# Kernel tuning notes

Measured on AMD Instinct MI355X. Metric: run time of the kernel, lower is better.

The kernel has to match this reference:

```python
import jax, jax.numpy as jnp
import numpy as np

B, S, D = 4, 2048, 512
H, DK, DV = 8, 64, 64

def setup_inputs() -> dict:
    key = jax.random.key(0)
    ks = jax.random.split(key, 11)
    s = 0.02
    return {
        "q_in": jax.random.normal(ks[0], (B, S, D), jnp.float32),
        "k_in": jax.random.normal(ks[1], (B, S, D), jnp.float32),
        "v_in": jax.random.normal(ks[2], (B, S, D), jnp.float32),
        "Wq": jax.random.normal(ks[3], (H, D, DK), jnp.float32) * s,
        "bq": jax.random.normal(ks[4], (H, DK), jnp.float32) * s,
        "Wk": jax.random.normal(ks[5], (H, D, DK), jnp.float32) * s,
        "bk": jax.random.normal(ks[6], (H, DK), jnp.float32) * s,
        "Wv": jax.random.normal(ks[7], (H, D, DV), jnp.float32) * s,
        "bv": jax.random.normal(ks[8], (H, DV), jnp.float32) * s,
        "Wo": jax.random.normal(ks[9], (H * DV, D), jnp.float32) * s,
        "bo": jax.random.normal(ks[10], (D,), jnp.float32) * s,
    }


def reference(q_in, k_in, v_in, Wq, bq, Wk, bk, Wv, bv, Wo, bo):
    # Per-head Q/K/V projections, batched over heads (same math as the
    # original Python loop over SingleAttention heads).
    q = jnp.einsum("bsd,hdk->bhsk", q_in, Wq) + bq[None, :, None, :]   # [B,H,S,DK]
    k = jnp.einsum("bsd,hdk->bhsk", k_in, Wk) + bk[None, :, None, :]   # [B,H,S,DK]
    v = jnp.einsum("bsd,hdv->bhsv", v_in, Wv) + bv[None, :, None, :]   # [B,H,S,DV]
    scale = 1.0 / jnp.sqrt(jnp.float32(DK))
    scores = jnp.einsum("bhqk,bhsk->bhqs", q, k) * scale               # [B,H,S,S]
    attn = jax.nn.softmax(scores, axis=-1)
    out = jnp.einsum("bhqs,bhsv->bhqv", attn, v)                        # [B,H,S,DV]
    # concat heads along feature dim: [B,S,H*DV]
    concat = out.transpose(0, 2, 1, 3).reshape(B, S, H * DV)
    return concat @ Wo + bo                                             # [B,S,D]
```

## Files before the change

kernel.cpp:

```cpp
#include <hip/hip_runtime.h>
#include <hip/hip_bf16.h>

using bf16 = __hip_bfloat16;
typedef short short8  __attribute__((ext_vector_type(8)));
typedef short short4v __attribute__((ext_vector_type(4)));
typedef float float4v __attribute__((ext_vector_type(4)));
typedef float f32x16  __attribute__((ext_vector_type(16)));
typedef unsigned int uint4v __attribute__((ext_vector_type(4)));

#define MFMA_BF16   __builtin_amdgcn_mfma_f32_16x16x32_bf16
#define MFMA32_BF16 __builtin_amdgcn_mfma_f32_32x32x16_bf16

#define B_  4
#define S_  2048
#define D_  512
#define H_  8
#define DK_ 64

__device__ __forceinline__ short f2bf(float f) {
  bf16 h = __float2bfloat16(f);
  return *reinterpret_cast<short*>(&h);
}

__device__ __forceinline__ unsigned cvtpk(float lo, float hi) {
  unsigned r;
  asm("v_cvt_pk_bf16_f32 %0, %1, %2" : "=v"(r) : "v"(lo), "v"(hi));
  return r;
}

__device__ __forceinline__ void plswap(unsigned& a, unsigned& b) {
  asm("v_permlane32_swap_b32 %0, %1" : "+v"(a), "+v"(b));
}

__device__ __forceinline__ short8 mk8(unsigned v0, unsigned v1, unsigned v2,
                                      unsigned v3) {
  uint4v u;
  u[0] = v0; u[1] = v1; u[2] = v2; u[3] = v3;
  return __builtin_bit_cast(short8, u);
}

#define GLL(g, l) __builtin_amdgcn_global_load_lds(                        \
      (const __attribute__((address_space(1))) void*)(g),                  \
      (__attribute__((address_space(3))) void*)(l), 16, 0, 0)

__global__ __launch_bounds__(256)
void prep(const float* __restrict__ qin, const float* __restrict__ kin,
          const float* __restrict__ vin, short* __restrict__ Xb,
          const float* __restrict__ Wq, const float* __restrict__ Wk,
          const float* __restrict__ Wv, const float* __restrict__ Wo,
          short* __restrict__ WqT, short* __restrict__ WkT,
          short* __restrict__ WvT, short* __restrict__ WoT) {
  __shared__ float tile[64 * 65];
  const int bid = blockIdx.x, tid = threadIdx.x;
  const size_t NTOK = (size_t)B_ * S_ * D_;

  if (bid < 6144) {
    const int z = bid >> 11, blk = bid & 2047;
    const float* src = (z == 0) ? qin : (z == 1) ? kin : vin;
    short* dst = Xb + (size_t)z * NTOK;
    const size_t base = ((size_t)blk * 256 + tid) * 8;
    float4v f0 = *(const float4v*)&src[base];
    float4v f1 = *(const float4v*)&src[base + 4];
    short8 s;
#pragma unroll
    for (int j = 0; j < 4; j++) { s[j] = f2bf(f0[j]); s[j + 4] = f2bf(f1[j]); }
    *(short8*)&dst[base] = s;
    return;
  }

  const int tw = bid - 6144;
  const int mat = tw >> 6, t = tw & 63;
  const float* W = (mat == 0) ? Wq : (mat == 1) ? Wk : (mat == 2) ? Wv : Wo;
  short* T       = (mat == 0) ? WqT : (mat == 1) ? WkT : (mat == 2) ? WvT : WoT;

  size_t sbase, ss, dbase;
  if (mat < 3) {
    int hh = t >> 3, d0 = (t & 7) * 64;
    sbase = (size_t)hh * 32768 + (size_t)d0 * 64;
    ss = 64;
    dbase = (size_t)hh * 64 * 512 + d0;
  } else {
    int n0 = (t >> 3) * 64, k0 = (t & 7) * 64;
    sbase = (size_t)k0 * 512 + n0;
    ss = 512;
    dbase = (size_t)n0 * 512 + k0;
  }

  {
    int r = tid >> 2, c0 = (tid & 3) * 16;
#pragma unroll
    for (int j = 0; j < 4; j++)
      *(float4v*)&tile[r * 65 + c0 + j * 4] =
          *(const float4v*)&W[sbase + (size_t)r * ss + c0 + j * 4];
  }
  __syncthreads();
  {
    int c = tid >> 2, r0 = (tid & 3) * 16;
#pragma unroll
    for (int j = 0; j < 2; j++) {
      short8 s;
#pragma unroll
      for (int u = 0; u < 8; u++) s[u] = f2bf(tile[(r0 + j * 8 + u) * 65 + c]);
      *(short8*)&T[dbase + (size_t)c * 512 + r0 + j * 8] = s;
    }
  }
}

__device__ __forceinline__ void gemm_core3(const short* __restrict__ A,
                                           const short* __restrict__ Bt,
                                           int m0, int n0,
                                           short* ABs,
                                           float4v acc[4][4]) {
  const int tid  = threadIdx.x;
  const int lane = tid & 63, wave = tid >> 6;
  const int quad = lane >> 4, l16 = lane & 15;
  const int wm = (wave >> 1) * 64, wn = (wave & 1) * 64;

  auto stage = [&](int buf, int k0) {
#pragma unroll
    for (int i = 0; i < 4; i++) {
      int q = (wave * 4 + i) * 64 + lane;
      int row = q >> 3, p = q & 7;
      int c = p ^ (row & 7);
      const short* src = (c < 4)
          ? &A [(size_t)(m0 + row) * 512 + k0 + c * 8]
          : &Bt[(size_t)(n0 + row) * 512 + k0 + (c - 4) * 8];
      GLL(src, &ABs[buf * 8192 + (wave * 4 + i) * 512]);
    }
  };
  auto comp = [&](int buf) {
    short8 af[4], bfr[4];
#pragma unroll
    for (int mi = 0; mi < 4; mi++) {
      int row = wm + mi * 16 + l16;
      af[mi] = *(short8*)&ABs[buf * 8192 + row * 64 + ((quad ^ (row & 7)) << 3)];
    }
#pragma unroll
    for (int ni = 0; ni < 4; ni++) {
      int row = wn + ni * 16 + l16;
      bfr[ni] = *(short8*)&ABs[buf * 8192 + row * 64 +
                               (((4 + quad) ^ (row & 7)) << 3)];
    }
#pragma unroll
    for (int mi = 0; mi < 4; mi++)
#pragma unroll
      for (int ni = 0; ni < 4; ni++)
        acc[mi][ni] = MFMA_BF16(af[mi], bfr[ni], acc[mi][ni], 0, 0, 0);
  };

  stage(0, 0);
  __syncthreads();
#pragma unroll
  for (int k = 0; k < 512; k += 64) {
    stage(1, k + 32);
    comp(0);
    __syncthreads();
    if (k + 64 < 512) stage(0, k + 64);
    comp(1);
    __syncthreads();
  }
}

__global__ __launch_bounds__(256, 4)
void qkv_gemm(const short* __restrict__ Xb,
              const short* __restrict__ WqT, const short* __restrict__ WkT,
              const short* __restrict__ WvT,
              const float* __restrict__ bq, const float* __restrict__ bk,
              const float* __restrict__ bv,
              short* __restrict__ Qp, short* __restrict__ Kp,
              short* __restrict__ Vt) {
  __shared__ __align__(16) short ABs[2 * 8192];
  const int m0 = blockIdx.x * 128, n0 = blockIdx.y * 128;
  const int z = blockIdx.z;
  const size_t NTOK = (size_t)B_ * S_ * D_;
  const short* A    = Xb + (size_t)z * NTOK;
  const short* Bt   = (z == 0) ? WqT : (z == 1) ? WkT : WvT;
  const float* bias = (z == 0) ? bq  : (z == 1) ? bk  : bv;
  const float scale = (z == 0) ? 0.125f * 1.44269504088896f : 1.0f;

  float4v acc[4][4];
#pragma unroll
  for (int mi = 0; mi < 4; mi++)
#pragma unroll
    for (int ni = 0; ni < 4; ni++) acc[mi][ni] = (float4v){0.f, 0.f, 0.f, 0.f};

  gemm_core3(A, Bt, m0, n0, ABs, acc);

  const int lane = threadIdx.x & 63, wave = threadIdx.x >> 6;
  const int quad = lane >> 4, l16 = lane & 15;
  const int wm = (wave >> 1) * 64, wn = (wave & 1) * 64;

  if (z < 2) {
    short* out = (z == 0) ? Qp : Kp;
#pragma unroll
    for (int mi = 0; mi < 4; mi++) {
      int m = m0 + wm + mi * 16 + quad * 4;
      int b = m >> 11, s = m & 2047;
#pragma unroll
      for (int ni = 0; ni < 4; ni++) {
        int n = n0 + wn + ni * 16 + l16;
        int h = n >> 6, dk = n & 63;
        float bb = bias[n];
        size_t base = (((size_t)b * H_ + h) * S_ + s) * 64 + dk;
#pragma unroll
        for (int r = 0; r < 4; r++)
          out[base + (size_t)r * 64] = f2bf((acc[mi][ni][r] + bb) * scale);
      }
    }
  } else {
#pragma unroll
    for (int mi = 0; mi < 4; mi++) {
      int m = m0 + wm + mi * 16 + quad * 4;
      int b = m >> 11, s = m & 2047;
#pragma unroll
      for (int ni = 0; ni < 4; ni++) {
        int n = n0 + wn + ni * 16 + l16;
        int h = n >> 6, v = n & 63;
        float bb = bias[n];
        short4v pk;
#pragma unroll
        for (int r = 0; r < 4; r++) pk[r] = f2bf(acc[mi][ni][r] + bb);
        *(short4v*)&Vt[(((size_t)b * H_ + h) * 64 + v) * S_ + s] = pk;
      }
    }
  }
}

__global__ __launch_bounds__(512, 4)
void attn_kernel(const short* __restrict__ Qp, const short* __restrict__ Kp,
                 const short* __restrict__ Vt, short* __restrict__ Ao) {
  __shared__ __align__(16) short sh[32768];

  const int orig = blockIdx.y * gridDim.x + blockIdx.x;
  const int lb = (orig & 7) * 64 + (orig >> 3);
  const int qt = lb & 15, bh = lb >> 4;
  const int b = bh >> 3, h = bh & 7;

  const int tid = threadIdx.x;
  const int lane = tid & 63, wave = tid >> 6;
  const int wg = wave & 3, half = wave >> 2;
  const int l31 = lane & 31, hi = lane >> 5, s7 = l31 & 7;

  const short* Qb = Qp + (size_t)bh * S_ * 64;
  const short* Kb = Kp + (size_t)bh * S_ * 64 + (size_t)half * 1024 * 64;
  const short* Vb = Vt + (size_t)bh * 64 * S_;

  short8 qf[4];
  {
    const short* qrow = Qb + (size_t)(qt * 128 + wg * 32 + l31) * 64;
#pragma unroll
    for (int w = 0; w < 4; w++)
      qf[w] = *(const short8*)&qrow[w * 16 + hi * 8];
  }

  const int slot0 = wg * 128 + lane;
  const int kr0 = slot0 >> 3, kc0 = slot0 & 7;
  const int kr1 = kr0 + 8;
  const short* kg0 = Kb + (size_t)kr0 * 64 + ((kc0 ^ (kr0 & 7)) << 3);
  const short* kg1 = Kb + (size_t)kr1 * 64 + ((kc0 ^ (kr1 & 7)) << 3);
  const short* vg0 = Vb + (size_t)kr0 * S_ + half * 1024 + ((kc0 ^ (kr0 & 7)) << 3);
  const short* vg1 = Vb + (size_t)kr1 * S_ + half * 1024 + ((kc0 ^ (kr1 & 7)) << 3);

  short* Kbase = sh;
  short* Vbase = sh + 16384;

  f32x16 acc0, acc1;
#pragma unroll
  for (int r = 0; r < 16; r++) { acc0[r] = 0.f; acc1[r] = 0.f; }
  float ls0 = 0.f, ls1 = 0.f;

  {
    short* kd = Kbase + (half * 2) * 4096 + wg * 1024;
    short* vd = Vbase + (half * 2) * 4096 + wg * 1024;
    GLL(kg0, kd); GLL(kg1, kd + 512);
    GLL(vg0, vd); GLL(vg1, vd + 512);
  }
  __syncthreads();

  for (int t = 0; t < 16; t++) {
    const int cur = t & 1;
    if (t < 15) {
      short* kd = Kbase + (half * 2 + (cur ^ 1)) * 4096 + wg * 1024;
      short* vd = Vbase + (half * 2 + (cur ^ 1)) * 4096 + wg * 1024;
      GLL(kg0 + (size_t)(t + 1) * 4096, kd);
      GLL(kg1 + (size_t)(t + 1) * 4096, kd + 512);
      GLL(vg0 + (size_t)(t + 1) * 64, vd);
      GLL(vg1 + (size_t)(t + 1) * 64, vd + 512);
    }
    const short* kb = Kbase + (half * 2 + cur) * 4096;
    const short* vs = Vbase + (half * 2 + cur) * 4096;

#pragma unroll
    for (int kt = 0; kt < 2; kt++) {
      f32x16 sa;
#pragma unroll
      for (int r = 0; r < 16; r++) sa[r] = 0.f;
      __builtin_amdgcn_s_setprio(1);
#pragma unroll
      for (int w = 0; w < 4; w++) {
        short8 kf = *(const short8*)&kb[(kt * 32 + l31) * 64 +
                                        (((2 * w + hi) ^ s7) << 3)];
        sa = MFMA32_BF16(kf, qf[w], sa, 0, 0, 0);
      }
      __builtin_amdgcn_s_setprio(0);

      float pv[16];
#pragma unroll
      for (int r = 0; r < 16; r++) pv[r] = exp2f(sa[r]);
#pragma unroll
      for (int r = 0; r < 8; r++) { ls0 += pv[r]; ls1 += pv[r + 8]; }

      unsigned a0 = cvtpk(pv[0], pv[1]),  b0 = cvtpk(pv[4], pv[5]);
      plswap(a0, b0);
      unsigned c0 = cvtpk(pv[2], pv[3]),  d0 = cvtpk(pv[6], pv[7]);
      plswap(c0, d0);
      short8 pa0 = mk8(a0, c0, b0, d0);
      unsigned a1 = cvtpk(pv[8], pv[9]),  b1 = cvtpk(pv[12], pv[13]);
      plswap(a1, b1);
      unsigned c1 = cvtpk(pv[10], pv[11]), d1 = cvtpk(pv[14], pv[15]);
      plswap(c1, d1);
      short8 pa1 = mk8(a1, c1, b1, d1);

      __builtin_amdgcn_s_setprio(1);
      {
        const int kw0 = kt * 2, kw1 = kt * 2 + 1;
        short8 v00 = *(const short8*)&vs[l31 * 64 + (((2 * kw0 + hi) ^ s7) << 3)];
        short8 v10 = *(const short8*)&vs[(32 + l31) * 64 + (((2 * kw0 + hi) ^ s7) << 3)];
        acc0 = MFMA32_BF16(pa0, v00, acc0, 0, 0, 0);
        acc1 = MFMA32_BF16(pa0, v10, acc1, 0, 0, 0);
        short8 v01 = *(const short8*)&vs[l31 * 64 + (((2 * kw1 + hi) ^ s7) << 3)];
        short8 v11 = *(const short8*)&vs[(32 + l31) * 64 + (((2 * kw1 + hi) ^ s7) << 3)];
        acc0 = MFMA32_BF16(pa1, v01, acc0, 0, 0, 0);
        acc1 = MFMA32_BF16(pa1, v11, acc1, 0, 0, 0);
      }
      __builtin_amdgcn_s_setprio(0);
    }
    __syncthreads();
  }

  float lsum = ls0 + ls1;
  lsum += __shfl_xor(lsum, 32, 64);

  float* fsh = (float*)sh;
  if (half == 1) {
    const int base = wg * 2304 + lane * 36;
#pragma unroll
    for (int r = 0; r < 16; r += 4) {
      *(float4v*)&fsh[base + r] =
          (float4v){acc0[r], acc0[r + 1], acc0[r + 2], acc0[r + 3]};
      *(float4v*)&fsh[base + 16 + r] =
          (float4v){acc1[r], acc1[r + 1], acc1[r + 2], acc1[r + 3]};
    }
    if (lane < 32) fsh[9216 + wg * 32 + l31] = lsum;
  }
  __syncthreads();
  if (half == 1) return;

  {
    const int base = wg * 2304 + lane * 36;
#pragma unroll
    for (int r = 0; r < 16; r += 4) {
      float4v u0 = *(float4v*)&fsh[base + r];
      acc0[r] += u0[0]; acc0[r + 1] += u0[1];
      acc0[r + 2] += u0[2]; acc0[r + 3] += u0[3];
      float4v u1 = *(float4v*)&fsh[base + 16 + r];
      acc1[r] += u1[0]; acc1[r + 1] += u1[1];
      acc1[r + 2] += u1[2]; acc1[r + 3] += u1[3];
    }
    lsum += fsh[9216 + wg * 32 + l31];
  }
  float myrl = 1.0f / lsum;

  const size_t obase =
      ((size_t)b * S_ + (size_t)(qt * 128 + wg * 32)) * D_ + h * 64 + l31;
#pragma unroll
  for (int r = 0; r < 16; r++) {
    int q = (r & 3) + 8 * (r >> 2) + 4 * hi;
    float rl = __shfl(myrl, q, 64);
    Ao[obase + (size_t)q * D_]      = f2bf(acc0[r] * rl);
    Ao[obase + (size_t)q * D_ + 32] = f2bf(acc1[r] * rl);
  }
}

__global__ __launch_bounds__(256, 4)
void out_gemm(const short* __restrict__ A, const short* __restrict__ Bt,
              const float* __restrict__ bias, float* __restrict__ out) {
  __shared__ __align__(16) short ABs[2 * 8192];
  const int m0 = blockIdx.x * 128, n0 = blockIdx.y * 128;

  float4v acc[4][4];
#pragma unroll
  for (int mi = 0; mi < 4; mi++)
#pragma unroll
    for (int ni = 0; ni < 4; ni++) acc[mi][ni] = (float4v){0.f, 0.f, 0.f, 0.f};

  gemm_core3(A, Bt, m0, n0, ABs, acc);

  const int lane = threadIdx.x & 63, wave = threadIdx.x >> 6;
  const int quad = lane >> 4, l16 = lane & 15;
  const int wm = (wave >> 1) * 64, wn = (wave & 1) * 64;
#pragma unroll
  for (int mi = 0; mi < 4; mi++) {
    int m = m0 + wm + mi * 16 + quad * 4;
#pragma unroll
    for (int ni = 0; ni < 4; ni++) {
      int n = n0 + wn + ni * 16 + l16;
      float bb = bias[n];
#pragma unroll
      for (int r = 0; r < 4; r++)
        out[(size_t)(m + r) * 512 + n] = acc[mi][ni][r] + bb;
    }
  }
}

extern "C" void kernel_launch(void* const* d_in, const int* in_sizes, int n_in,
                              void* d_out, int out_size, void* d_ws, size_t ws_size,
                              hipStream_t stream) {
  const float* qin = (const float*)d_in[0];
  const float* kin = (const float*)d_in[1];
  const float* vin = (const float*)d_in[2];
  const float* Wq  = (const float*)d_in[3];
  const float* bq  = (const float*)d_in[4];
  const float* Wk  = (const float*)d_in[5];
  const float* bk  = (const float*)d_in[6];
  const float* Wv  = (const float*)d_in[7];
  const float* bv  = (const float*)d_in[8];
  const float* Wo  = (const float*)d_in[9];
  const float* bo  = (const float*)d_in[10];
  float* out = (float*)d_out;
  short* ws  = (short*)d_ws;

  const size_t NTOK = (size_t)B_ * S_ * D_;
  short* Qp  = ws;
  short* Kp  = ws + NTOK;
  short* Vt  = ws + 2 * NTOK;
  short* Ao  = ws + 3 * NTOK;
  short* WqT = ws + 4 * NTOK;
  short* WkT = WqT + 512 * 512;
  short* WvT = WkT + 512 * 512;
  short* WoT = WvT + 512 * 512;
  short* Xb  = WoT + 512 * 512;

  prep<<<dim3(6400), 256, 0, stream>>>(qin, kin, vin, Xb, Wq, Wk, Wv, Wo,
                                       WqT, WkT, WvT, WoT);
  qkv_gemm<<<dim3(64, 4, 3), 256, 0, stream>>>(Xb, WqT, WkT, WvT,
                                               bq, bk, bv, Qp, Kp, Vt);
  attn_kernel<<<dim3(16, 32), 512, 0, stream>>>(Qp, Kp, Vt, Ao);
  out_gemm<<<dim3(64, 4), 256, 0, stream>>>(Ao, WoT, bo, out);
}
```

Measured before the change: 190.3 us.

## Compute softmax row sums via MFMA with ones and transpose V projection GEMM

The attention kernel now gets the softmax denominator from an extra MFMA that multiplies the bf16 probabilities by a vector of ones, replacing the per-lane scalar adds and the cross-lane shuffles. The sums therefore come from the same bf16-rounded probabilities used in the PV product, at the cost of two more MFMAs per tile. The V projection GEMM is also transposed (weights as A, activations as B), so results land in the V-transposed layout with scalar stores along the sequence dimension.

```diff
diff --git a/kernel.cpp b/kernel.cpp
--- a/kernel.cpp
+++ b/kernel.cpp
@@ -170,11 +170,12 @@
               short* __restrict__ Qp, short* __restrict__ Kp,
               short* __restrict__ Vt) {
   __shared__ __align__(16) short ABs[2 * 8192];
-  const int m0 = blockIdx.x * 128, n0 = blockIdx.y * 128;
   const int z = blockIdx.z;
+  const int m0 = (z == 2) ? blockIdx.y * 128 : blockIdx.x * 128;
+  const int n0 = (z == 2) ? blockIdx.x * 128 : blockIdx.y * 128;
   const size_t NTOK = (size_t)B_ * S_ * D_;
-  const short* A    = Xb + (size_t)z * NTOK;
-  const short* Bt   = (z == 0) ? WqT : (z == 1) ? WkT : WvT;
+  const short* A    = (z == 2) ? WvT : Xb + (size_t)z * NTOK;
+  const short* Bt   = (z == 0) ? WqT : (z == 1) ? WkT : Xb + 2 * NTOK;
   const float* bias = (z == 0) ? bq  : (z == 1) ? bk  : bv;
   const float scale = (z == 0) ? 0.125f * 1.44269504088896f : 1.0f;
 
@@ -211,16 +212,18 @@
 #pragma unroll
     for (int mi = 0; mi < 4; mi++) {
       int m = m0 + wm + mi * 16 + quad * 4;
-      int b = m >> 11, s = m & 2047;
-#pragma unroll
-      for (int ni = 0; ni < 4; ni++) {
-        int n = n0 + wn + ni * 16 + l16;
-        int h = n >> 6, v = n & 63;
-        float bb = bias[n];
-        short4v pk;
-#pragma unroll
-        for (int r = 0; r < 4; r++) pk[r] = f2bf(acc[mi][ni][r] + bb);
-        *(short4v*)&Vt[(((size_t)b * H_ + h) * 64 + v) * S_ + s] = pk;
+#pragma unroll
+      for (int r = 0; r < 4; r++) {
+        int hv = m + r;
+        int h = hv >> 6, v = hv & 63;
+        float bb = bias[hv];
+#pragma unroll
+        for (int ni = 0; ni < 4; ni++) {
+          int n = n0 + wn + ni * 16 + l16;
+          int b = n >> 11, sl = n & 2047;
+          Vt[(((size_t)b * H_ + h) * 64 + v) * S_ + sl] =
+              f2bf(acc[mi][ni][r] + bb);
+        }
       }
     }
   }
@@ -252,6 +255,10 @@
     for (int w = 0; w < 4; w++)
       qf[w] = *(const short8*)&qrow[w * 16 + hi * 8];
   }
+
+  short8 ones8;
+#pragma unroll
+  for (int j = 0; j < 8; j++) ones8[j] = (short)0x3F80;
 
   const int slot0 = wg * 128 + lane;
   const int kr0 = slot0 >> 3, kc0 = slot0 & 7;
@@ -264,10 +271,9 @@
   short* Kbase = sh;
   short* Vbase = sh + 16384;
 
-  f32x16 acc0, acc1;
-#pragma unroll
-  for (int r = 0; r < 16; r++) { acc0[r] = 0.f; acc1[r] = 0.f; }
-  float ls0 = 0.f, ls1 = 0.f;
+  f32x16 acc0, acc1, accl;
+#pragma unroll
+  for (int r = 0; r < 16; r++) { acc0[r] = 0.f; acc1[r] = 0.f; accl[r] = 0.f; }
 
   {
     short* kd = Kbase + (half * 2) * 4096 + wg * 1024;
@@ -307,8 +313,6 @@
       float pv[16];
 #pragma unroll
       for (int r = 0; r < 16; r++) pv[r] = exp2f(sa[r]);
-#pragma unroll
-      for (int r = 0; r < 8; r++) { ls0 += pv[r]; ls1 += pv[r + 8]; }
 
       unsigned a0 = cvtpk(pv[0], pv[1]),  b0 = cvtpk(pv[4], pv[5]);
       plswap(a0, b0);
@@ -322,6 +326,8 @@
       short8 pa1 = mk8(a1, c1, b1, d1);
 
       __builtin_amdgcn_s_setprio(1);
+      accl = MFMA32_BF16(pa0, ones8, accl, 0, 0, 0);
+      accl = MFMA32_BF16(pa1, ones8, accl, 0, 0, 0);
       {
         const int kw0 = kt * 2, kw1 = kt * 2 + 1;
         short8 v00 = *(const short8*)&vs[l31 * 64 + (((2 * kw0 + hi) ^ s7) << 3)];
@@ -338,9 +344,6 @@
     __syncthreads();
   }
 
-  float lsum = ls0 + ls1;
-  lsum += __shfl_xor(lsum, 32, 64);
-
   float* fsh = (float*)sh;
   if (half == 1) {
     const int base = wg * 2304 + lane * 36;
@@ -351,7 +354,11 @@
       *(float4v*)&fsh[base + 16 + r] =
           (float4v){acc1[r], acc1[r + 1], acc1[r + 2], acc1[r + 3]};
     }
-    if (lane < 32) fsh[9216 + wg * 32 + l31] = lsum;
+    if (l31 == 0) {
+#pragma unroll
+      for (int r = 0; r < 16; r++)
+        fsh[9216 + wg * 32 + (r & 3) + 8 * (r >> 2) + 4 * hi] = accl[r];
+    }
   }
   __syncthreads();
   if (half == 1) return;
@@ -367,16 +374,17 @@
       acc1[r] += u1[0]; acc1[r + 1] += u1[1];
       acc1[r + 2] += u1[2]; acc1[r + 3] += u1[3];
     }
-    lsum += fsh[9216 + wg * 32 + l31];
-  }
-  float myrl = 1.0f / lsum;
+#pragma unroll
+    for (int r = 0; r < 16; r++)
+      accl[r] += fsh[9216 + wg * 32 + (r & 3) + 8 * (r >> 2) + 4 * hi];
+  }
 
   const size_t obase =
       ((size_t)b * S_ + (size_t)(qt * 128 + wg * 32)) * D_ + h * 64 + l31;
 #pragma unroll
   for (int r = 0; r < 16; r++) {
     int q = (r & 3) + 8 * (r >> 2) + 4 * hi;
-    float rl = __shfl(myrl, q, 64);
+    float rl = 1.0f / accl[r];
     Ao[obase + (size_t)q * D_]      = f2bf(acc0[r] * rl);
     Ao[obase + (size_t)q * D_ + 32] = f2bf(acc1[r] * rl);
   }
```

Measured after the change: 193.8 us. About the same (+1.8%).
